# Kernel optimization log

Hardware: AMD Instinct MI355X
Metric: run time of the kernel (lower is better)

## Reference

```python
import jax, jax.numpy as jnp
import numpy as np

# XORChainModel.forward: state[0] = inputs[0]; state[i] = state[i-1] ^ inputs[i]
# i.e. a cumulative XOR (inclusive prefix scan with XOR) along the chain axis.
# XOR is associative, so we use jax.lax.associative_scan (log-depth parallel scan).

SEQ_LEN = 4096  # number of steps in the XOR chain (len(inputs) list in torch)
BITS = 8192     # self.bits: width of each bit vector


def setup_inputs() -> dict:
    key = jax.random.key(0)
    # inputs[i] is a 1-D bit vector of length BITS; stack the whole list into [S, BITS]
    inputs = jax.random.randint(key, (SEQ_LEN, BITS), 0, 2, dtype=jnp.int32)
    return {"inputs": inputs}


def reference(inputs):
    # outputs[i] = inputs[0] ^ inputs[1] ^ ... ^ inputs[i]
    # Equivalent to the torch module's list of per-step states, stacked on axis 0.
    return jax.lax.associative_scan(jnp.bitwise_xor, inputs, axis=0)
```

## Files before the change

### kernel.cpp

```cpp
#include <hip/hip_runtime.h>


#define S 4096
#define B4 2048
#define CHUNK 64
#define NCHUNK (S / CHUNK)
#define TPB 256
#define NCT (B4 / TPB)
#define NBLK (NCHUNK * NCT)
#define NWORDS (NCHUNK * B4)

typedef unsigned int v4u __attribute__((ext_vector_type(4)));

__device__ __forceinline__ unsigned pack4(v4u v) {
    return (v.x & 1u) | ((v.y & 1u) << 1) | ((v.z & 1u) << 2) | ((v.w & 1u) << 3);
}
__device__ __forceinline__ bool valid(unsigned w) {
    return (w & 0x300u) == 0x100u;
}

__global__ __launch_bounds__(64) void ctl_init(unsigned* __restrict__ w) {
    w[threadIdx.x] = 0u;
}

__global__ __launch_bounds__(TPB, 4) void xor_lookback2(
        const v4u* __restrict__ in, v4u* __restrict__ out,
        unsigned* __restrict__ ctl) {
    unsigned* agg = ctl + 64;
    unsigned* inc = agg + NWORDS;

    __shared__ unsigned sh_t;
    const int tid = threadIdx.x;
    if (tid == 0) sh_t = atomicAdd(&ctl[0], 1u);
    __syncthreads();
    const unsigned t = sh_t;
    const int ct    = (int)(t & (NCT - 1));
    const int chunk = (int)(t >> 3);
    const int colg  = ct * TPB + tid;

    const v4u* p = in + (size_t)chunk * CHUNK * B4 + colg;

    v4u acc = (v4u){0u, 0u, 0u, 0u};
#pragma unroll
    for (int g = 0; g < CHUNK / 16; ++g) {
        v4u v[16];
#pragma unroll
        for (int j = 0; j < 16; ++j) v[j] = p[(size_t)(g * 16 + j) * B4];
#pragma unroll
        for (int j = 0; j < 16; ++j) acc ^= v[j];
    }
    const unsigned myagg = pack4(acc);
    __hip_atomic_store(&agg[(size_t)chunk * B4 + colg], 0x100u | myagg,
                       __ATOMIC_RELAXED, __HIP_MEMORY_SCOPE_AGENT);

    unsigned ex = 0u;
    int k = chunk - 1;
    while (k >= 0) {
        unsigned iw = __hip_atomic_load(&inc[(size_t)k * B4 + colg],
                                        __ATOMIC_RELAXED,
                                        __HIP_MEMORY_SCOPE_AGENT);
        if (valid(iw)) { ex ^= (iw & 0xFu); break; }
        int n = (k + 1 < 16) ? (k + 1) : 16;
        unsigned a[16];
        for (int j = 0; j < n; ++j)
            a[j] = __hip_atomic_load(&agg[(size_t)(k - j) * B4 + colg],
                                     __ATOMIC_RELAXED,
                                     __HIP_MEMORY_SCOPE_AGENT);
        int consumed = 0;
        for (int j = 0; j < n; ++j) {
            if (valid(a[j])) { ex ^= (a[j] & 0xFu); ++consumed; }
            else break;
        }
        k -= consumed;
        if (consumed == 0) __builtin_amdgcn_s_sleep(2);
    }
    __hip_atomic_store(&inc[(size_t)chunk * B4 + colg], 0x100u | (ex ^ myagg),
                       __ATOMIC_RELAXED, __HIP_MEMORY_SCOPE_AGENT);

    v4u run = (v4u){ex & 1u, (ex >> 1) & 1u, (ex >> 2) & 1u, (ex >> 3) & 1u};
    v4u* q = out + (size_t)chunk * CHUNK * B4 + colg;
#pragma unroll
    for (int g = 0; g < CHUNK / 16; ++g) {
        v4u v[16];
#pragma unroll
        for (int j = 0; j < 16; ++j) v[j] = p[(size_t)(g * 16 + j) * B4];
#pragma unroll
        for (int j = 0; j < 16; ++j) {
            run ^= v[j];
            __builtin_nontemporal_store(run, &q[(size_t)(g * 16 + j) * B4]);
        }
    }
}

extern "C" void kernel_launch(void* const* d_in, const int* in_sizes, int n_in,
                              void* d_out, int out_size, void* d_ws, size_t ws_size,
                              hipStream_t stream) {
    const v4u* in = (const v4u*)d_in[0];
    v4u* out = (v4u*)d_out;
    unsigned* ctl = (unsigned*)d_ws;

    ctl_init<<<1, 64, 0, stream>>>(ctl);
    xor_lookback2<<<NBLK, TPB, 0, stream>>>(in, out, ctl);
}
```

Baseline: 256.1 us.

## Stage local prefix in LDS to avoid rereading input, shrink chunk size

Each block now computes the within-chunk inclusive prefix in registers and stages it in shared memory. After the decoupled look-back it writes seed XOR staged values, so the second global read of the input chunk goes away. The chunk shrinks from 64 to 16 rows, which gives 4x more blocks and a longer look-back chain, and the spin sleep is shortened. The trade is more look-back traffic and serialization risk in exchange for half the global read traffic.

```diff
diff --git a/kernel.cpp b/kernel.cpp
--- a/kernel.cpp
+++ b/kernel.cpp
@@ -3,7 +3,7 @@
 
 #define S 4096
 #define B4 2048
-#define CHUNK 64
+#define CHUNK 16
 #define NCHUNK (S / CHUNK)
 #define TPB 256
 #define NCT (B4 / TPB)
@@ -23,9 +23,10 @@
     w[threadIdx.x] = 0u;
 }
 
-__global__ __launch_bounds__(TPB, 4) void xor_lookback2(
+__global__ __launch_bounds__(TPB, 2) void xor_lookback3(
         const v4u* __restrict__ in, v4u* __restrict__ out,
         unsigned* __restrict__ ctl) {
+    extern __shared__ v4u lds[];
     unsigned* agg = ctl + 64;
     unsigned* inc = agg + NWORDS;
 
@@ -40,16 +41,15 @@
 
     const v4u* p = in + (size_t)chunk * CHUNK * B4 + colg;
 
-    v4u acc = (v4u){0u, 0u, 0u, 0u};
+    v4u v[CHUNK];
 #pragma unroll
-    for (int g = 0; g < CHUNK / 16; ++g) {
-        v4u v[16];
+    for (int r = 0; r < CHUNK; ++r) v[r] = p[(size_t)r * B4];
 #pragma unroll
-        for (int j = 0; j < 16; ++j) v[j] = p[(size_t)(g * 16 + j) * B4];
+    for (int r = 1; r < CHUNK; ++r) v[r] ^= v[r - 1];
 #pragma unroll
-        for (int j = 0; j < 16; ++j) acc ^= v[j];
-    }
-    const unsigned myagg = pack4(acc);
+    for (int r = 0; r < CHUNK; ++r) lds[r * TPB + tid] = v[r];
+
+    const unsigned myagg = pack4(v[CHUNK - 1]);
     __hip_atomic_store(&agg[(size_t)chunk * B4 + colg], 0x100u | myagg,
                        __ATOMIC_RELAXED, __HIP_MEMORY_SCOPE_AGENT);
 
@@ -72,23 +72,17 @@
             else break;
         }
         k -= consumed;
-        if (consumed == 0) __builtin_amdgcn_s_sleep(2);
+        if (consumed == 0) __builtin_amdgcn_s_sleep(1);
     }
     __hip_atomic_store(&inc[(size_t)chunk * B4 + colg], 0x100u | (ex ^ myagg),
                        __ATOMIC_RELAXED, __HIP_MEMORY_SCOPE_AGENT);
 
-    v4u run = (v4u){ex & 1u, (ex >> 1) & 1u, (ex >> 2) & 1u, (ex >> 3) & 1u};
+    v4u seed = (v4u){ex & 1u, (ex >> 1) & 1u, (ex >> 2) & 1u, (ex >> 3) & 1u};
     v4u* q = out + (size_t)chunk * CHUNK * B4 + colg;
 #pragma unroll
-    for (int g = 0; g < CHUNK / 16; ++g) {
-        v4u v[16];
-#pragma unroll
-        for (int j = 0; j < 16; ++j) v[j] = p[(size_t)(g * 16 + j) * B4];
-#pragma unroll
-        for (int j = 0; j < 16; ++j) {
-            run ^= v[j];
-            __builtin_nontemporal_store(run, &q[(size_t)(g * 16 + j) * B4]);
-        }
+    for (int r = 0; r < CHUNK; ++r) {
+        v4u w = lds[r * TPB + tid];
+        __builtin_nontemporal_store(seed ^ w, &q[(size_t)r * B4]);
     }
 }
 
@@ -100,5 +94,6 @@
     unsigned* ctl = (unsigned*)d_ws;
 
     ctl_init<<<1, 64, 0, stream>>>(ctl);
-    xor_lookback2<<<NBLK, TPB, 0, stream>>>(in, out, ctl);
+    xor_lookback3<<<NBLK, TPB, (size_t)CHUNK * TPB * sizeof(v4u), stream>>>(
+        in, out, ctl);
 }
```

After: 246.3 us. -3.8%, faster.
